# Kernel tuning notes

Hardware: AMD Instinct MI355X
Metric: run time of the kernel (lower is better)

## Reference

```python
import jax, jax.numpy as jnp
import numpy as np

B, W, N = 4, 8, 1024
F_IN, HID, OUT = 256, 256, 128


def setup_inputs() -> dict:
    key = jax.random.key(0)
    ks = jax.random.split(key, 8)
    X = jax.random.normal(ks[0], (B, W, N, F_IN), dtype=jnp.float32)
    adj = jax.random.uniform(ks[1], (B, W, N, N), dtype=jnp.float32)
    # Linear params, torch default init: U(-1/sqrt(fan_in), 1/sqrt(fan_in))
    def lin(k, fi, fo):
        k1, k2 = jax.random.split(k)
        bnd = 1.0 / np.sqrt(fi)
        Wm = jax.random.uniform(k1, (fi, fo), minval=-bnd, maxval=bnd, dtype=jnp.float32)
        bm = jax.random.uniform(k2, (fo,), minval=-bnd, maxval=bnd, dtype=jnp.float32)
        return Wm, bm
    W1, b1 = lin(ks[2], F_IN, HID)
    W2, b2 = lin(ks[3], HID, HID)
    W3, b3 = lin(ks[4], HID, OUT)
    return {"X": X, "adj": adj, "W1": W1, "b1": b1, "W2": W2, "b2": b2, "W3": W3, "b3": b3}


def _normalize(adj):
    # adj: [B, W, N, N]. adj_hat = adj + I; sym degree norm D^-1/2 A D^-1/2
    n = adj.shape[-1]
    adj_hat = adj + jnp.eye(n, dtype=adj.dtype)
    d = jnp.sum(adj_hat, axis=-1) ** (-0.5)            # [B, W, N]
    # diag(d) @ adj_hat @ diag(d) == row/col scaling (same math, no N^3 diag matmuls)
    return adj_hat * d[..., :, None] * d[..., None, :]


def reference(X, adj, W1, b1, W2, b2, W3, b3):
    adj_norm = _normalize(adj)                          # [B, W, N, N]
    h = X
    for Wm, bm in ((W1, b1), (W2, b2), (W3, b3)):
        h = jnp.einsum('bwnm,bwmf->bwnf', adj_norm, h)  # aggregate
        h = jax.nn.relu(jnp.einsum('bwnf,fo->bwno', h, Wm) + bm)
    return h                                            # [B, W, N, OUT]
```

## Files before the change

### kernel.cpp

```cpp
#include <hip/hip_runtime.h>
#include <hip/hip_bf16.h>
#include <cstdint>
#include <cstddef>

#define NN 1024
#define FF 256

typedef __attribute__((ext_vector_type(8))) short bf16x8;
typedef __attribute__((ext_vector_type(4))) float f32x4;

typedef __attribute__((address_space(1))) const void* gas_ptr;
typedef __attribute__((address_space(3))) void* las_ptr;

__device__ __forceinline__ short f2bf(float x) {
  unsigned int u = __float_as_uint(x);
  u = (u + 0x7fffu + ((u >> 16) & 1u)) >> 16;
  return (short)u;
}


__global__ __launch_bounds__(256)
void dinv_cast(const float* __restrict__ adj, float* __restrict__ dinv,
               short* __restrict__ Ahat) {
  __shared__ float wsum[64];
  int b = blockIdx.x;
  int bw = b >> 6, s = b & 63;
  int t = threadIdx.x;
  int wid = t >> 6, lane = t & 63;
  int row = lane & 15;
  int rloc = (s << 4) + row;
  int kg = (lane >> 4) & 3;
  const float* arow = adj + ((size_t)(bw << 10) + rloc) * NN;
  short* outb = Ahat + ((size_t)bw << 20) + ((size_t)s << 14) + (t << 3);
  float ssum = 0.f;
  #pragma unroll
  for (int it = 0; it < 8; it++) {
    int col = (it << 7) + (wid << 5) + (kg << 3);
    float4 a0 = *(const float4*)(arow + col);
    float4 a1 = *(const float4*)(arow + col + 4);
    float v[8] = {a0.x, a0.y, a0.z, a0.w, a1.x, a1.y, a1.z, a1.w};
    union { ushort o[8]; int4 q; } pk;
    #pragma unroll
    for (int j = 0; j < 8; j++) {
      v[j] += (rloc == col + j) ? 1.f : 0.f;
      ssum += v[j];
      pk.o[j] = (ushort)f2bf(v[j]);
    }
    *(int4*)(outb + (it << 11)) = pk.q;
  }
  ssum += __shfl_down(ssum, 32, 64);
  ssum += __shfl_down(ssum, 16, 64);
  if (lane < 16) wsum[(wid << 4) + lane] = ssum;
  __syncthreads();
  if (t < 16) {
    float tot = wsum[t] + wsum[16 + t] + wsum[32 + t] + wsum[48 + t];
    dinv[(bw << 10) + (s << 4) + t] = rsqrtf(tot);
  }
}

__global__ __launch_bounds__(256)
void preproc_xw(const float* __restrict__ X, const float* __restrict__ dinv,
                short* __restrict__ XT,
                const float* __restrict__ W1, const float* __restrict__ W2,
                const float* __restrict__ W3,
                short* __restrict__ T1, short* __restrict__ T2,
                short* __restrict__ T3) {
  __shared__ short T[64][72];
  int b = blockIdx.x;
  int t = threadIdx.x;
  if (b < 2048) {
    int bwo = b >> 6;
    int n0 = (b & 15) << 6, f0 = ((b >> 4) & 3) << 6;
    {
      int n = t >> 2, fc = (t & 3) << 4;
      float dn = dinv[(bwo << 10) + n0 + n];
      const float* src = X + (((size_t)bwo * NN + n0 + n) * FF) + f0 + fc;
      #pragma unroll
      for (int i = 0; i < 4; i++) {
        float4 v = ((const float4*)src)[i];
        ushort4 p;
        p.x = (unsigned short)f2bf(v.x * dn); p.y = (unsigned short)f2bf(v.y * dn);
        p.z = (unsigned short)f2bf(v.z * dn); p.w = (unsigned short)f2bf(v.w * dn);
        *(ushort4*)&T[n][fc + (i << 2)] = p;
      }
    }
    __syncthreads();
    {
      int f = t >> 2, nc = (t & 3) << 4;
      int fg = f0 + f, ng = n0 + nc;
      short tmp[16];
      #pragma unroll
      for (int i = 0; i < 16; i++) tmp[i] = T[nc + i][f];
      size_t e0 = ((size_t)bwo << 18) + ((size_t)(fg >> 4) << 14) + ((ng >> 5) << 9)
                + (((ng & 31) >> 3) << 7) + ((fg & 15) << 3);
      *(int4*)(XT + e0)       = *(int4*)&tmp[0];
      *(int4*)(XT + e0 + 128) = *(int4*)&tmp[8];
    }
  } else {
    int idx = (b - 2048) * 256 + t;
    const float* W; short* Td; int FO; int loc;
    if (idx < 65536)       { W = W1; Td = T1; FO = 256; loc = idx; }
    else if (idx < 131072) { W = W2; Td = T2; FO = 256; loc = idx - 65536; }
    else                   { W = W3; Td = T3; FO = 128; loc = idx - 131072; }
    int fo = loc >> 8, fi = loc & 255;
    if (fo < FO) {
      size_t e = (size_t)((fo >> 4) << 12) + ((fi >> 5) << 9)
               + (((fi & 31) >> 3) << 7) + ((fo & 15) << 3) + (fi & 7);
      Td[e] = f2bf(W[fi * FO + fo]);
    }
  }
}

template<int F_OUT, bool FINAL>
__global__ __launch_bounds__(512)
void gcn_layer(const short* __restrict__ Ahat,
               const float* __restrict__ dinv,
               const short* __restrict__ Gin,
               const short* __restrict__ WT,
               const float* __restrict__ bias,
               short* __restrict__ Gout,
               float* __restrict__ Out) {
  __shared__ __align__(16) short lds[73728];

  int b = blockIdx.x;
  int x = b & 7, m = b >> 3;
  int bw = (x << 2) + (m >> 3);
  int rb = m & 7;
  int r0 = rb << 7;

  int tid = threadIdx.x;
  int wid = tid >> 6, lane = tid & 63;
  int l15 = lane & 15, l4 = lane >> 4;
  int wr = wid >> 2, wf = wid & 3;

  const float* dvB = dinv + (bw << 10);
  const short* Abase = Ahat + ((size_t)bw << 20) + ((size_t)(rb << 3) << 14);
  const short* Hbase = Gin + ((size_t)bw << 18);

  auto stage3 = [&](int sel, int t, int half) {
    char* base = (char*)lds + sel * 49152;
    int kb = t << 1;
    #pragma unroll
    for (int i = 0; i < 3; i++) {
      int j = half * 3 + i;
      int slot = (j << 9) + tid;
      const short* g;
      if (j < 2) {
        int c = slot >> 6, o = slot & 63;
        g = Abase + ((size_t)(c >> 1) << 14) + ((size_t)(kb + (c & 1)) << 9) + (o << 3);
      } else {
        int s2 = slot - 1024;
        int c = s2 >> 6, o = s2 & 63;
        g = Hbase + ((size_t)(c >> 1) << 14) + ((size_t)(kb + (c & 1)) << 9) + (o << 3);
      }
      __builtin_amdgcn_global_load_lds((gas_ptr)g, (las_ptr)(base + (slot << 4)), 16, 0, 0);
    }
  };

  f32x4 acc[4][4];
  #pragma unroll
  for (int ah = 0; ah < 4; ah++)
    #pragma unroll
    for (int aa = 0; aa < 4; aa++) acc[ah][aa] = f32x4{0.f, 0.f, 0.f, 0.f};

  stage3(0, 0, 0); stage3(0, 0, 1);
  stage3(1, 1, 0); stage3(1, 1, 1);
  asm volatile("s_waitcnt vmcnt(6)" ::: "memory");
  __builtin_amdgcn_sched_barrier(0);
  __builtin_amdgcn_s_barrier();

  #pragma unroll
  for (int t = 0; t < 16; ++t) {
    const char* base = (const char*)lds + (t % 3) * 49152;
    #pragma unroll
    for (int p = 0; p < 2; ++p) {
      if (t <= 13) stage3((t + 2) % 3, t + 2, p);
      bf16x8 aT[4], hT[4];
      #pragma unroll
      for (int aa = 0; aa < 4; aa++) {
        int c = (((wr << 2) + aa) << 1) + p;
        aT[aa] = *(const bf16x8*)(base + (c << 10) + (lane << 4));
      }
      #pragma unroll
      for (int ah = 0; ah < 4; ah++) {
        int c = (((wf << 2) + ah) << 1) + p;
        hT[ah] = *(const bf16x8*)(base + 16384 + (c << 10) + (lane << 4));
      }
      __builtin_amdgcn_s_barrier();
      asm volatile("s_waitcnt lgkmcnt(0)" ::: "memory");
      __builtin_amdgcn_sched_barrier(0);
      __builtin_amdgcn_s_setprio(1);
      #pragma unroll
      for (int ah = 0; ah < 4; ah++)
        #pragma unroll
        for (int aa = 0; aa < 4; aa++)
          acc[ah][aa] = __builtin_amdgcn_mfma_f32_16x16x32_bf16(
              hT[ah], aT[aa], acc[ah][aa], 0, 0, 0);
      __builtin_amdgcn_s_setprio(0);
      if (p == 1 && t <= 13) {
        asm volatile("s_waitcnt vmcnt(6)" ::: "memory");
        __builtin_amdgcn_sched_barrier(0);
      } else if (p == 1 && t == 14) {
        asm volatile("s_waitcnt vmcnt(0)" ::: "memory");
        __builtin_amdgcn_sched_barrier(0);
      }
      __builtin_amdgcn_s_barrier();
    }
  }

  short* aggL = lds;
  float dsc[4];
  #pragma unroll
  for (int aa = 0; aa < 4; aa++) dsc[aa] = dvB[r0 + (wr << 6) + (aa << 4) + l15];
  #pragma unroll
  for (int ah = 0; ah < 4; ah++)
    #pragma unroll
    for (int aa = 0; aa < 4; aa++) {
      int r = (wr << 6) + (aa << 4) + l15;
      int fB = ((wf << 6) + (ah << 4) + (l4 << 2)) << 1;
      int off = (r * 544 + (fB ^ ((r & 7) << 4))) >> 1;
      ushort4 p;
      p.x = (unsigned short)f2bf(acc[ah][aa][0] * dsc[aa]);
      p.y = (unsigned short)f2bf(acc[ah][aa][1] * dsc[aa]);
      p.z = (unsigned short)f2bf(acc[ah][aa][2] * dsc[aa]);
      p.w = (unsigned short)f2bf(acc[ah][aa][3] * dsc[aa]);
      *(ushort4*)(aggL + off) = p;
    }
  __syncthreads();

  constexpr int NFO = F_OUT / 64;
  const short* Wbase = WT + (size_t)(wf * NFO) * 4096 + (lane << 3);
  f32x4 acc2[4][NFO];
  #pragma unroll
  for (int am = 0; am < 4; am++)
    #pragma unroll
    for (int nf = 0; nf < NFO; nf++) acc2[am][nf] = f32x4{0.f, 0.f, 0.f, 0.f};

  #pragma unroll
  for (int kt = 0; kt < 8; kt++) {
    bf16x8 af[4];
    #pragma unroll
    for (int am = 0; am < 4; am++) {
      int r = (wr << 6) + (am << 4) + l15;
      int fB = (kt << 6) + (l4 << 4);
      af[am] = *(const bf16x8*)(aggL + ((r * 544 + (fB ^ ((r & 7) << 4))) >> 1));
    }
    #pragma unroll
    for (int nf = 0; nf < NFO; nf++) {
      bf16x8 wv = *(const bf16x8*)(Wbase + (size_t)nf * 4096 + (kt << 9));
      #pragma unroll
      for (int am = 0; am < 4; am++)
        acc2[am][nf] = __builtin_amdgcn_mfma_f32_16x16x32_bf16(af[am], wv, acc2[am][nf], 0, 0, 0);
    }
  }

  #pragma unroll
  for (int am = 0; am < 4; am++) {
    int nodeLoc = (wr << 6) + (am << 4) + (l4 << 2);
    float4 dn4 = *(const float4*)(dvB + r0 + nodeLoc);
    float dn[4] = {dn4.x, dn4.y, dn4.z, dn4.w};
    #pragma unroll
    for (int nf = 0; nf < NFO; nf++) {
      int fo = wf * (F_OUT / 4) + (nf << 4) + l15;
      float bb = bias[fo];
      float v[4];
      #pragma unroll
      for (int j = 0; j < 4; j++) v[j] = fmaxf(acc2[am][nf][j] + bb, 0.f);
      if (!FINAL) {
        ushort4 p;
        p.x = (unsigned short)f2bf(v[0] * dn[0]);
        p.y = (unsigned short)f2bf(v[1] * dn[1]);
        p.z = (unsigned short)f2bf(v[2] * dn[2]);
        p.w = (unsigned short)f2bf(v[3] * dn[3]);
        size_t e = (size_t)bw * (F_OUT * 1024) + ((size_t)(fo >> 4) << 14)
                 + ((size_t)((rb << 2) + (wr << 1) + (am >> 1)) << 9)
                 + ((size_t)(((am & 1) << 1) + (l4 >> 1)) << 7)
                 + ((fo & 15) << 3) + ((l4 & 1) << 2);
        *(ushort4*)(Gout + e) = p;
      } else {
        float* ob = Out + ((size_t)(bw << 10) + r0 + nodeLoc) * F_OUT + fo;
        ob[0]         = v[0];
        ob[F_OUT]     = v[1];
        ob[2 * F_OUT] = v[2];
        ob[3 * F_OUT] = v[3];
      }
    }
  }
}

extern "C" void kernel_launch(void* const* d_in, const int* in_sizes, int n_in,
                              void* d_out, int out_size, void* d_ws, size_t ws_size,
                              hipStream_t stream) {
  const float* X   = (const float*)d_in[0];
  const float* adj = (const float*)d_in[1];
  const float* W1  = (const float*)d_in[2];
  const float* b1  = (const float*)d_in[3];
  const float* W2  = (const float*)d_in[4];
  const float* b2  = (const float*)d_in[5];
  const float* W3  = (const float*)d_in[6];
  const float* b3  = (const float*)d_in[7];
  float* out = (float*)d_out;

  char* ws = (char*)d_ws;
  float* dinv = (float*)ws;
  short* WT1  = (short*)(ws + 131072);
  short* WT2  = (short*)(ws + 262144);
  short* WT3  = (short*)(ws + 393216);
  short* bufA = (short*)(ws + 458752);
  short* bufB = (short*)(ws + 458752 + 16777216);
  short* Ahat = (short*)(ws + 458752 + 2 * 16777216);

  dinv_cast<<<2048, 256, 0, stream>>>(adj, dinv, Ahat);
  preproc_xw<<<2688, 256, 0, stream>>>(X, dinv, bufA, W1, W2, W3, WT1, WT2, WT3);

  gcn_layer<256, false><<<256, 512, 0, stream>>>(Ahat, dinv, bufA, WT1, b1, bufB, nullptr);
  gcn_layer<256, false><<<256, 512, 0, stream>>>(Ahat, dinv, bufB, WT2, b2, bufA, nullptr);
  gcn_layer<128, true ><<<256, 512, 0, stream>>>(Ahat, dinv, bufA, WT3, b3, nullptr, out);
}
```

Measured before the change: 130.7 us.

## Load H operand directly from global, stage only A tiles in LDS double buffer

The aggregation GEMM no longer stages the H (features) tile through LDS. Each wave reads its H fragments directly from global memory into registers, and only the adjacency tile goes through LDS, now as a two-stage double buffer with larger 64KB stages and fewer barriers. The degree/cast kernel also issues all its row loads up front before reducing, to expose more memory parallelism. This trades LDS traffic and barrier count for direct global (L2) reads of H, repeated across waves. It also brings a full vmcnt(0) wait per stage that may expose latency.

```diff
diff --git a/kernel.cpp b/kernel.cpp
--- a/kernel.cpp
+++ b/kernel.cpp
@@ -32,13 +32,19 @@
   int kg = (lane >> 4) & 3;
   const float* arow = adj + ((size_t)(bw << 10) + rloc) * NN;
   short* outb = Ahat + ((size_t)bw << 20) + ((size_t)s << 14) + (t << 3);
-  float ssum = 0.f;
+  float4 va[16];
   #pragma unroll
   for (int it = 0; it < 8; it++) {
     int col = (it << 7) + (wid << 5) + (kg << 3);
-    float4 a0 = *(const float4*)(arow + col);
-    float4 a1 = *(const float4*)(arow + col + 4);
-    float v[8] = {a0.x, a0.y, a0.z, a0.w, a1.x, a1.y, a1.z, a1.w};
+    va[2 * it]     = *(const float4*)(arow + col);
+    va[2 * it + 1] = *(const float4*)(arow + col + 4);
+  }
+  float ssum = 0.f;
+  #pragma unroll
+  for (int it = 0; it < 8; it++) {
+    int col = (it << 7) + (wid << 5) + (kg << 3);
+    float v[8] = {va[2*it].x, va[2*it].y, va[2*it].z, va[2*it].w,
+                  va[2*it+1].x, va[2*it+1].y, va[2*it+1].z, va[2*it+1].w};
     union { ushort o[8]; int4 q; } pk;
     #pragma unroll
     for (int j = 0; j < 8; j++) {
@@ -120,7 +126,7 @@
                const float* __restrict__ bias,
                short* __restrict__ Gout,
                float* __restrict__ Out) {
-  __shared__ __align__(16) short lds[73728];
+  __shared__ __align__(16) short lds[65536];
 
   int b = blockIdx.x;
   int x = b & 7, m = b >> 3;
@@ -135,24 +141,17 @@
 
   const float* dvB = dinv + (bw << 10);
   const short* Abase = Ahat + ((size_t)bw << 20) + ((size_t)(rb << 3) << 14);
-  const short* Hbase = Gin + ((size_t)bw << 18);
-
-  auto stage3 = [&](int sel, int t, int half) {
-    char* base = (char*)lds + sel * 49152;
-    int kb = t << 1;
-    #pragma unroll
-    for (int i = 0; i < 3; i++) {
-      int j = half * 3 + i;
-      int slot = (j << 9) + tid;
-      const short* g;
-      if (j < 2) {
-        int c = slot >> 6, o = slot & 63;
-        g = Abase + ((size_t)(c >> 1) << 14) + ((size_t)(kb + (c & 1)) << 9) + (o << 3);
-      } else {
-        int s2 = slot - 1024;
-        int c = s2 >> 6, o = s2 & 63;
-        g = Hbase + ((size_t)(c >> 1) << 14) + ((size_t)(kb + (c & 1)) << 9) + (o << 3);
-      }
+  const short* Hb = Gin + ((size_t)bw << 18) + ((size_t)(wf << 2) << 14) + (lane << 3);
+
+  auto stageSS = [&](int sel, int ss) {
+    char* base = (char*)lds + (sel << 16);
+    #pragma unroll
+    for (int i = 0; i < 8; i++) {
+      int slot = (i << 9) + tid;
+      int c = slot >> 6, o = slot & 63;
+      int s_ = c >> 3, kk = c & 7;
+      const short* g = Abase + ((size_t)s_ << 14)
+                     + ((size_t)((ss << 3) + kk) << 9) + (o << 3);
       __builtin_amdgcn_global_load_lds((gas_ptr)g, (las_ptr)(base + (slot << 4)), 16, 0, 0);
     }
   };
@@ -163,49 +162,43 @@
     #pragma unroll
     for (int aa = 0; aa < 4; aa++) acc[ah][aa] = f32x4{0.f, 0.f, 0.f, 0.f};
 
-  stage3(0, 0, 0); stage3(0, 0, 1);
-  stage3(1, 1, 0); stage3(1, 1, 1);
-  asm volatile("s_waitcnt vmcnt(6)" ::: "memory");
+  stageSS(0, 0);
+  asm volatile("s_waitcnt vmcnt(0)" ::: "memory");
   __builtin_amdgcn_sched_barrier(0);
   __builtin_amdgcn_s_barrier();
 
-  #pragma unroll
-  for (int t = 0; t < 16; ++t) {
-    const char* base = (const char*)lds + (t % 3) * 49152;
-    #pragma unroll
-    for (int p = 0; p < 2; ++p) {
-      if (t <= 13) stage3((t + 2) % 3, t + 2, p);
-      bf16x8 aT[4], hT[4];
+  for (int ss = 0; ss < 4; ++ss) {
+    if (ss < 3) stageSS((ss + 1) & 1, ss + 1);
+    const char* base = (const char*)lds + ((ss & 1) << 16);
+    #pragma unroll
+    for (int tl = 0; tl < 4; ++tl) {
+      bf16x8 h[4][2], aT[4][2];
+      #pragma unroll
+      for (int ah = 0; ah < 4; ah++) {
+        int kg = (ss << 3) + (tl << 1);
+        h[ah][0] = *(const bf16x8*)(Hb + ah * 16384 + (size_t)kg * 512);
+        h[ah][1] = *(const bf16x8*)(Hb + ah * 16384 + (size_t)(kg + 1) * 512);
+      }
       #pragma unroll
       for (int aa = 0; aa < 4; aa++) {
-        int c = (((wr << 2) + aa) << 1) + p;
-        aT[aa] = *(const bf16x8*)(base + (c << 10) + (lane << 4));
+        int s_ = (wr << 2) + aa;
+        aT[aa][0] = *(const bf16x8*)(base + (((s_ << 3) + (tl << 1)) << 10) + (lane << 4));
+        aT[aa][1] = *(const bf16x8*)(base + (((s_ << 3) + (tl << 1) + 1) << 10) + (lane << 4));
       }
-      #pragma unroll
-      for (int ah = 0; ah < 4; ah++) {
-        int c = (((wf << 2) + ah) << 1) + p;
-        hT[ah] = *(const bf16x8*)(base + 16384 + (c << 10) + (lane << 4));
-      }
-      __builtin_amdgcn_s_barrier();
-      asm volatile("s_waitcnt lgkmcnt(0)" ::: "memory");
-      __builtin_amdgcn_sched_barrier(0);
       __builtin_amdgcn_s_setprio(1);
       #pragma unroll
-      for (int ah = 0; ah < 4; ah++)
+      for (int kt = 0; kt < 2; kt++)
         #pragma unroll
-        for (int aa = 0; aa < 4; aa++)
-          acc[ah][aa] = __builtin_amdgcn_mfma_f32_16x16x32_bf16(
-              hT[ah], aT[aa], acc[ah][aa], 0, 0, 0);
+        for (int ah = 0; ah < 4; ah++)
+          #pragma unroll
+          for (int aa = 0; aa < 4; aa++)
+            acc[ah][aa] = __builtin_amdgcn_mfma_f32_16x16x32_bf16(
+                h[ah][kt], aT[aa][kt], acc[ah][aa], 0, 0, 0);
       __builtin_amdgcn_s_setprio(0);
-      if (p == 1 && t <= 13) {
-        asm volatile("s_waitcnt vmcnt(6)" ::: "memory");
-        __builtin_amdgcn_sched_barrier(0);
-      } else if (p == 1 && t == 14) {
-        asm volatile("s_waitcnt vmcnt(0)" ::: "memory");
-        __builtin_amdgcn_sched_barrier(0);
-      }
-      __builtin_amdgcn_s_barrier();
-    }
+    }
+    asm volatile("s_waitcnt vmcnt(0)" ::: "memory");
+    __builtin_amdgcn_sched_barrier(0);
+    __builtin_amdgcn_s_barrier();
   }
 
   short* aggL = lds;
```

After: 141.9 us. 1.09x slower.
